# Kernel tuning notes

Measured on AMD Instinct MI355X. Metric: run time of the kernel, lower is better.

Reference implementation:

```python
import jax, jax.numpy as jnp
import numpy as np

N_GAUSS = 512
PLANE = 512


def setup_inputs() -> dict:
    key = jax.random.key(0)
    k1, k2, k3, k4, k5 = jax.random.split(key, 5)
    mean = jax.random.uniform(k1, (N_GAUSS, 2, 1), dtype=jnp.float32)
    alpha = jax.random.uniform(k2, (N_GAUSS, 1), dtype=jnp.float32)
    scale = jax.random.uniform(k3, (N_GAUSS, 2), dtype=jnp.float32)
    theta = jax.random.uniform(k4, (N_GAUSS, 1), dtype=jnp.float32)
    rgb = jax.random.uniform(k5, (N_GAUSS, 3), dtype=jnp.float32)
    # render plane: torch.meshgrid(x, y, indexing='xy'), stack([x, y], -1)
    lin = jnp.linspace(0.0, 1.0, PLANE, dtype=jnp.float32)
    xx, yy = jnp.meshgrid(lin, lin, indexing='xy')
    pixels = jnp.stack([xx, yy], axis=-1)  # (H, W, 2)
    return {"mean": mean, "alpha": alpha, "scale": scale, "theta": theta,
            "rgb": rgb, "pixels": pixels}


def _forward(mean, alpha, scale, theta, rgb, pixels):
    two_pi = 2.0 * jnp.pi
    # covariance = R S S^T R^T with R from circular_activation(theta)
    ta = two_pi * theta                      # (N,1)
    c = jnp.cos(ta)
    s = jnp.sin(ta)
    rot = jnp.stack([jnp.concatenate([c, -s], axis=-1),
                     jnp.concatenate([s, c], axis=-1)], axis=-2)   # (N,2,2)
    smat = jnp.eye(2, dtype=scale.dtype)[None] * scale[..., None]  # (N,2,2)
    cov = rot @ smat @ jnp.swapaxes(smat, -1, -2) @ jnp.swapaxes(rot, -1, -2)
    a = cov[:, 0, 0]
    b01 = cov[:, 0, 1]
    b10 = cov[:, 1, 0]
    d = cov[:, 1, 1]
    det = a * d - b01 * b10                  # (N,)
    inv00 = d / det
    inv01 = -b01 / det
    inv10 = -b10 / det
    inv11 = a / det
    # quadratic form per pixel (analytic 2x2, same math as diff^T inv diff)
    mu = mean[:, :, 0]                       # (N,2)
    dx = pixels[None, :, :, 0] - mu[:, 0][:, None, None]  # (N,H,W)
    dy = pixels[None, :, :, 1] - mu[:, 1][:, None, None]  # (N,H,W)
    q = (inv00[:, None, None] * dx * dx
         + (inv01 + inv10)[:, None, None] * dx * dy
         + inv11[:, None, None] * dy * dy)
    prob = jnp.exp(-0.5 * q) / (two_pi * jnp.sqrt(det))[:, None, None]  # (N,H,W)
    splat = prob / jnp.max(prob)             # global max-normalize
    weighted = rgb * alpha                   # (N,3) rgb * alpha mask
    img = jnp.einsum('nhw,nc->hwc', splat, weighted)  # sum over gaussians
    return jax.nn.sigmoid(img)               # (H,W,3)


def reference(mean, alpha, scale, theta, rgb, pixels):
    return _forward(mean, alpha, scale, theta, rgb, pixels)
```

## Files before the change

kernel.cpp:

```cpp
#include <hip/hip_runtime.h>

#define NG 512
#define PLANE 512

typedef float v2f __attribute__((ext_vector_type(2)));

#define PRM_OFF  16
#define SLOT_OFF 4352

__global__ __launch_bounds__(256) void prep_kernel(
    const float* __restrict__ mean, const float* __restrict__ alpha,
    const float* __restrict__ scale, const float* __restrict__ theta,
    const float* __restrict__ rgb, float* __restrict__ ws) {
    const int n   = blockIdx.x;
    const int tid = threadIdx.x;

    const float TWO_PI = 6.283185307179586f;
    float th = theta[n];
    float c = __builtin_amdgcn_cosf(th);
    float s = __builtin_amdgcn_sinf(th);
    float sx = scale[2 * n], sy = scale[2 * n + 1];

    float m200 = (c * sx) * sx;
    float m201 = (-(s * sy)) * sy;
    float m210 = (s * sx) * sx;
    float m211 = (c * sy) * sy;
    float a   = m200 * c + m201 * (-s);
    float b01 = m200 * s + m201 * c;
    float b10 = m210 * c + m211 * (-s);
    float d   = m210 * s + m211 * c;

    float det = a * d - b01 * b10;
    float rdet = __builtin_amdgcn_rcpf(det);
    float inv00 = d * rdet;
    float inv01 = -b01 * rdet;
    float inv10 = -b10 * rdet;
    float inv11 = a * rdet;

    float norm = __builtin_amdgcn_rcpf(TWO_PI * __builtin_amdgcn_sqrtf(det));
    const float K = -0.5f * 1.4426950408889634f;

    float A_ = K * inv00;
    float B_ = K * (inv01 + inv10);
    float C_ = K * inv11;
    float mx = mean[2 * n], my = mean[2 * n + 1];
    float Lg = fmaf(-0.5f, __builtin_amdgcn_logf(det), -2.651496129472319f);

    if (tid == 0) {
        float w = alpha[n] * norm;
        float4* p = (float4*)(ws + PRM_OFF + 8 * n);
        p[0] = make_float4(A_, B_, C_, mx);
        p[1] = make_float4(my, w * rgb[3 * n], w * rgb[3 * n + 1], w * rgb[3 * n + 2]);
    }

    const float STEP = 1.0f / 511.0f;
    float inv2A = __builtin_amdgcn_rcpf(2.0f * A_);
    float t = -1e30f;
#pragma unroll
    for (int k = 0; k < 2; ++k) {
        int r = tid + (k << 8);
        float y  = (float)r * STEP;
        float dy = y - my;
        float bdy  = B_ * dy;
        float cdy2 = C_ * (dy * dy);
        float xstar = mx - bdy * inv2A;
        float xs = fminf(fmaxf(xstar, 0.0f), 1.0f);
        int i1 = min((int)(xs * 511.0f), 510);
#pragma unroll
        for (int kk = -1; kk <= 2; ++kk) {
            int i = max(0, min(i1 + kk, 511));
            float x = (float)i * STEP;
            float dx = x - mx;
            float q = fmaf(fmaf(A_, dx, bdy), dx, cdy2);
            t = fmaxf(t, q);
        }
    }
    t += Lg;

#pragma unroll
    for (int off = 32; off > 0; off >>= 1)
        t = fmaxf(t, __shfl_xor(t, off));
    __shared__ float sm[4];
    if ((tid & 63) == 0) sm[tid >> 6] = t;
    __syncthreads();
    if (tid == 0) {
        float mm = fmaxf(fmaxf(sm[0], sm[1]), fmaxf(sm[2], sm[3]));
        ws[SLOT_OFF + n] = mm;
    }
}

__global__ __launch_bounds__(256, 8) void splat_kernel(
    const float* __restrict__ pixels, const float* __restrict__ ws,
    float* __restrict__ out) {
    const int tid  = threadIdx.x;
    const int wv   = __builtin_amdgcn_readfirstlane(tid >> 6);
    const int lane = tid & 63;
    const int pair = blockIdx.x * 64 + lane;
    const int row  = pair >> 8;
    const int col0 = (pair & 255) << 1;
    const int pbase = row * PLANE + col0;

    float4 pix = *reinterpret_cast<const float4*>(pixels + 2 * pbase);
    const float y = pix.y;
    const v2f xx = {pix.x, pix.z};

    const float4* prm4 = reinterpret_cast<const float4*>(ws + PRM_OFF) + (wv << 8);

    v2f accr = {0.f, 0.f}, accg = {0.f, 0.f}, accb = {0.f, 0.f};

    float4 pa = prm4[0];
    float4 pb = prm4[1];
#pragma unroll 4
    for (int n = 0; n < 128; ++n) {
        float4 na = prm4[2 * n + 2];
        float4 nb = prm4[2 * n + 3];

        float a = pa.x, b = pa.y, cc = pa.z, mx = pa.w;
        float my = pb.x, wr = pb.y, wg = pb.z, wb = pb.w;

        float dy   = y - my;
        float bdy  = b * dy;
        float cdy2 = cc * (dy * dy);

        v2f dx = xx - (v2f){mx, mx};
        v2f t  = __builtin_elementwise_fma(dx, (v2f){a, a}, (v2f){bdy, bdy});
        v2f q  = __builtin_elementwise_fma(t, dx, (v2f){cdy2, cdy2});

        v2f e = {__builtin_amdgcn_exp2f(q.x), __builtin_amdgcn_exp2f(q.y)};

        accr = __builtin_elementwise_fma(e, (v2f){wr, wr}, accr);
        accg = __builtin_elementwise_fma(e, (v2f){wg, wg}, accg);
        accb = __builtin_elementwise_fma(e, (v2f){wb, wb}, accb);

        pa = na; pb = nb;
    }

    __shared__ float red[4][64][7];
    red[wv][lane][0] = accr.x; red[wv][lane][1] = accg.x; red[wv][lane][2] = accb.x;
    red[wv][lane][3] = accr.y; red[wv][lane][4] = accg.y; red[wv][lane][5] = accb.y;
    __syncthreads();

    if (wv == 0) {
        float v0 = red[0][lane][0] + red[1][lane][0] + red[2][lane][0] + red[3][lane][0];
        float v1 = red[0][lane][1] + red[1][lane][1] + red[2][lane][1] + red[3][lane][1];
        float v2 = red[0][lane][2] + red[1][lane][2] + red[2][lane][2] + red[3][lane][2];
        float v3 = red[0][lane][3] + red[1][lane][3] + red[2][lane][3] + red[3][lane][3];
        float v4 = red[0][lane][4] + red[1][lane][4] + red[2][lane][4] + red[3][lane][4];
        float v5 = red[0][lane][5] + red[1][lane][5] + red[2][lane][5] + red[3][lane][5];

        const float4* sl = reinterpret_cast<const float4*>(ws + SLOT_OFF) + 2 * lane;
        float4 s0 = sl[0], s1 = sl[1];
        float m = fmaxf(fmaxf(fmaxf(s0.x, s0.y), fmaxf(s0.z, s0.w)),
                        fmaxf(fmaxf(s1.x, s1.y), fmaxf(s1.z, s1.w)));
#pragma unroll
        for (int off = 32; off > 0; off >>= 1)
            m = fmaxf(m, __shfl_xor(m, off));
        float invmax = __builtin_amdgcn_exp2f(-m);

        const float KE = 1.4426950408889634f;
        v0 *= invmax; v1 *= invmax; v2 *= invmax;
        v3 *= invmax; v4 *= invmax; v5 *= invmax;
        v0 = __builtin_amdgcn_rcpf(1.0f + __builtin_amdgcn_exp2f(-KE * v0));
        v1 = __builtin_amdgcn_rcpf(1.0f + __builtin_amdgcn_exp2f(-KE * v1));
        v2 = __builtin_amdgcn_rcpf(1.0f + __builtin_amdgcn_exp2f(-KE * v2));
        v3 = __builtin_amdgcn_rcpf(1.0f + __builtin_amdgcn_exp2f(-KE * v3));
        v4 = __builtin_amdgcn_rcpf(1.0f + __builtin_amdgcn_exp2f(-KE * v4));
        v5 = __builtin_amdgcn_rcpf(1.0f + __builtin_amdgcn_exp2f(-KE * v5));

        float* o = out + (size_t)pbase * 3;
        *reinterpret_cast<float2*>(o + 0) = make_float2(v0, v1);
        *reinterpret_cast<float2*>(o + 2) = make_float2(v2, v3);
        *reinterpret_cast<float2*>(o + 4) = make_float2(v4, v5);
    }
}

extern "C" void kernel_launch(void* const* d_in, const int* in_sizes, int n_in,
                              void* d_out, int out_size, void* d_ws, size_t ws_size,
                              hipStream_t stream) {
    const float* mean   = (const float*)d_in[0];
    const float* alpha  = (const float*)d_in[1];
    const float* scale  = (const float*)d_in[2];
    const float* theta  = (const float*)d_in[3];
    const float* rgb    = (const float*)d_in[4];
    const float* pixels = (const float*)d_in[5];
    float* out = (float*)d_out;
    float* ws  = (float*)d_ws;

    prep_kernel<<<512, 256, 0, stream>>>(mean, alpha, scale, theta, rgb, ws);

    splat_kernel<<<2048, 256, 0, stream>>>(pixels, ws, out);
}
```

Before: 95.42 us.

## Process four pixels per lane and split gaussians across eight waves

```diff
diff --git a/kernel.cpp b/kernel.cpp
--- a/kernel.cpp
+++ b/kernel.cpp
@@ -89,31 +89,30 @@
     }
 }
 
-__global__ __launch_bounds__(256, 8) void splat_kernel(
+__global__ __launch_bounds__(512, 4) void splat_kernel(
     const float* __restrict__ pixels, const float* __restrict__ ws,
     float* __restrict__ out) {
     const int tid  = threadIdx.x;
     const int wv   = __builtin_amdgcn_readfirstlane(tid >> 6);
     const int lane = tid & 63;
-    const int pair = blockIdx.x * 64 + lane;
-    const int row  = pair >> 8;
-    const int col0 = (pair & 255) << 1;
-    const int pbase = row * PLANE + col0;
+    const int quad = blockIdx.x * 64 + lane;
+    const int pbase = quad << 2;
 
-    float4 pix = *reinterpret_cast<const float4*>(pixels + 2 * pbase);
-    const float y = pix.y;
-    const v2f xx = {pix.x, pix.z};
+    float4 p01 = *reinterpret_cast<const float4*>(pixels + 2 * pbase);
+    float4 p23 = *reinterpret_cast<const float4*>(pixels + 2 * pbase + 4);
+    const float y = p01.y;
+    const v2f x01 = {p01.x, p01.z};
+    const v2f x23 = {p23.x, p23.z};
 
-    const float4* prm4 = reinterpret_cast<const float4*>(ws + PRM_OFF) + (wv << 8);
+    const float4* prm4 = reinterpret_cast<const float4*>(ws + PRM_OFF) + (wv << 7);
 
-    v2f accr = {0.f, 0.f}, accg = {0.f, 0.f}, accb = {0.f, 0.f};
+    v2f ar01 = {0.f, 0.f}, ag01 = {0.f, 0.f}, ab01 = {0.f, 0.f};
+    v2f ar23 = {0.f, 0.f}, ag23 = {0.f, 0.f}, ab23 = {0.f, 0.f};
 
-    float4 pa = prm4[0];
-    float4 pb = prm4[1];
-#pragma unroll 4
-    for (int n = 0; n < 128; ++n) {
-        float4 na = prm4[2 * n + 2];
-        float4 nb = prm4[2 * n + 3];
+#pragma unroll 8
+    for (int n = 0; n < 64; ++n) {
+        float4 pa = prm4[2 * n];
+        float4 pb = prm4[2 * n + 1];
 
         float a = pa.x, b = pa.y, cc = pa.z, mx = pa.w;
         float my = pb.x, wr = pb.y, wg = pb.z, wb = pb.w;
@@ -121,33 +120,34 @@
         float dy   = y - my;
         float bdy  = b * dy;
         float cdy2 = cc * (dy * dy);
+        v2f bdyv  = {bdy, bdy};
+        v2f cdy2v = {cdy2, cdy2};
 
-        v2f dx = xx - (v2f){mx, mx};
-        v2f t  = __builtin_elementwise_fma(dx, (v2f){a, a}, (v2f){bdy, bdy});
-        v2f q  = __builtin_elementwise_fma(t, dx, (v2f){cdy2, cdy2});
+        v2f dx01 = x01 - (v2f){mx, mx};
+        v2f dx23 = x23 - (v2f){mx, mx};
+        v2f t01 = __builtin_elementwise_fma(dx01, (v2f){a, a}, bdyv);
+        v2f t23 = __builtin_elementwise_fma(dx23, (v2f){a, a}, bdyv);
+        v2f q01 = __builtin_elementwise_fma(t01, dx01, cdy2v);
+        v2f q23 = __builtin_elementwise_fma(t23, dx23, cdy2v);
 
-        v2f e = {__builtin_amdgcn_exp2f(q.x), __builtin_amdgcn_exp2f(q.y)};
+        v2f e01 = {__builtin_amdgcn_exp2f(q01.x), __builtin_amdgcn_exp2f(q01.y)};
+        v2f e23 = {__builtin_amdgcn_exp2f(q23.x), __builtin_amdgcn_exp2f(q23.y)};
 
-        accr = __builtin_elementwise_fma(e, (v2f){wr, wr}, accr);
-        accg = __builtin_elementwise_fma(e, (v2f){wg, wg}, accg);
-        accb = __builtin_elementwise_fma(e, (v2f){wb, wb}, accb);
-
-        pa = na; pb = nb;
+        ar01 = __builtin_elementwise_fma(e01, (v2f){wr, wr}, ar01);
+        ag01 = __builtin_elementwise_fma(e01, (v2f){wg, wg}, ag01);
+        ab01 = __builtin_elementwise_fma(e01, (v2f){wb, wb}, ab01);
+        ar23 = __builtin_elementwise_fma(e23, (v2f){wr, wr}, ar23);
+        ag23 = __builtin_elementwise_fma(e23, (v2f){wg, wg}, ag23);
+        ab23 = __builtin_elementwise_fma(e23, (v2f){wb, wb}, ab23);
     }
 
-    __shared__ float red[4][64][7];
-    red[wv][lane][0] = accr.x; red[wv][lane][1] = accg.x; red[wv][lane][2] = accb.x;
-    red[wv][lane][3] = accr.y; red[wv][lane][4] = accg.y; red[wv][lane][5] = accb.y;
-    __syncthreads();
+    __shared__ float4 red[8][64][3];
+    red[wv][lane][0] = make_float4(ar01.x, ag01.x, ab01.x, ar01.y);
+    red[wv][lane][1] = make_float4(ag01.y, ab01.y, ar23.x, ag23.x);
+    red[wv][lane][2] = make_float4(ab23.x, ar23.y, ag23.y, ab23.y);
 
+    float invmax = 0.f;
     if (wv == 0) {
-        float v0 = red[0][lane][0] + red[1][lane][0] + red[2][lane][0] + red[3][lane][0];
-        float v1 = red[0][lane][1] + red[1][lane][1] + red[2][lane][1] + red[3][lane][1];
-        float v2 = red[0][lane][2] + red[1][lane][2] + red[2][lane][2] + red[3][lane][2];
-        float v3 = red[0][lane][3] + red[1][lane][3] + red[2][lane][3] + red[3][lane][3];
-        float v4 = red[0][lane][4] + red[1][lane][4] + red[2][lane][4] + red[3][lane][4];
-        float v5 = red[0][lane][5] + red[1][lane][5] + red[2][lane][5] + red[3][lane][5];
-
         const float4* sl = reinterpret_cast<const float4*>(ws + SLOT_OFF) + 2 * lane;
         float4 s0 = sl[0], s1 = sl[1];
         float m = fmaxf(fmaxf(fmaxf(s0.x, s0.y), fmaxf(s0.z, s0.w)),
@@ -155,22 +155,29 @@
 #pragma unroll
         for (int off = 32; off > 0; off >>= 1)
             m = fmaxf(m, __shfl_xor(m, off));
-        float invmax = __builtin_amdgcn_exp2f(-m);
+        invmax = __builtin_amdgcn_exp2f(-m);
+    }
+    __syncthreads();
+
+    if (wv == 0) {
+        float4 v0 = red[0][lane][0], v1 = red[0][lane][1], v2 = red[0][lane][2];
+#pragma unroll
+        for (int cch = 1; cch < 8; ++cch) {
+            float4 u0 = red[cch][lane][0], u1 = red[cch][lane][1], u2 = red[cch][lane][2];
+            v0.x += u0.x; v0.y += u0.y; v0.z += u0.z; v0.w += u0.w;
+            v1.x += u1.x; v1.y += u1.y; v1.z += u1.z; v1.w += u1.w;
+            v2.x += u2.x; v2.y += u2.y; v2.z += u2.z; v2.w += u2.w;
+        }
 
         const float KE = 1.4426950408889634f;
-        v0 *= invmax; v1 *= invmax; v2 *= invmax;
-        v3 *= invmax; v4 *= invmax; v5 *= invmax;
-        v0 = __builtin_amdgcn_rcpf(1.0f + __builtin_amdgcn_exp2f(-KE * v0));
-        v1 = __builtin_amdgcn_rcpf(1.0f + __builtin_amdgcn_exp2f(-KE * v1));
-        v2 = __builtin_amdgcn_rcpf(1.0f + __builtin_amdgcn_exp2f(-KE * v2));
-        v3 = __builtin_amdgcn_rcpf(1.0f + __builtin_amdgcn_exp2f(-KE * v3));
-        v4 = __builtin_amdgcn_rcpf(1.0f + __builtin_amdgcn_exp2f(-KE * v4));
-        v5 = __builtin_amdgcn_rcpf(1.0f + __builtin_amdgcn_exp2f(-KE * v5));
+#define SIG(x) __builtin_amdgcn_rcpf(1.0f + __builtin_amdgcn_exp2f(-KE * ((x) * invmax)))
+        v0.x = SIG(v0.x); v0.y = SIG(v0.y); v0.z = SIG(v0.z); v0.w = SIG(v0.w);
+        v1.x = SIG(v1.x); v1.y = SIG(v1.y); v1.z = SIG(v1.z); v1.w = SIG(v1.w);
+        v2.x = SIG(v2.x); v2.y = SIG(v2.y); v2.z = SIG(v2.z); v2.w = SIG(v2.w);
+#undef SIG
 
-        float* o = out + (size_t)pbase * 3;
-        *reinterpret_cast<float2*>(o + 0) = make_float2(v0, v1);
-        *reinterpret_cast<float2*>(o + 2) = make_float2(v2, v3);
-        *reinterpret_cast<float2*>(o + 4) = make_float2(v4, v5);
+        float4* o = reinterpret_cast<float4*>(out + (size_t)pbase * 3);
+        o[0] = v0; o[1] = v1; o[2] = v2;
     }
 }
 
@@ -188,5 +195,5 @@
 
     prep_kernel<<<512, 256, 0, stream>>>(mean, alpha, scale, theta, rgb, ws);
 
-    splat_kernel<<<2048, 256, 0, stream>>>(pixels, ws, out);
+    splat_kernel<<<1024, 512, 0, stream>>>(pixels, ws, out);
 }
```

Result: faster. 90.16 us (-5.5%).
